# Kernel optimization log

Hardware: AMD Instinct MI355X
Metric: run time of the kernel (lower is better)

Reference implementation:

```python
import jax, jax.numpy as jnp
import numpy as np

NUM_QUERIES = 900
EMBED_DIM = 256
NUM_HEADS = 8
EPS = 1e-5


def bilinear_sample(feats, grid):
    """F.grid_sample(..., align_corners=False, padding_mode='zeros', bilinear).
    feats: [BN, C, H, W], grid: [BN, Q, 2] in [-1,1] (x, y). Returns [BN, Q, C]."""
    BN, C, H, W = feats.shape
    ix = (grid[..., 0] + 1.0) * (W * 0.5) - 0.5
    iy = (grid[..., 1] + 1.0) * (H * 0.5) - 0.5
    x0 = jnp.floor(ix)
    y0 = jnp.floor(iy)
    wx1 = ix - x0
    wy1 = iy - y0
    x0i = x0.astype(jnp.int32)
    y0i = y0.astype(jnp.int32)
    x1i = x0i + 1
    y1i = y0i + 1
    b = jnp.arange(BN)[:, None]

    def gather(yy, xx):
        inb = (xx >= 0) & (xx < W) & (yy >= 0) & (yy < H)
        yc = jnp.clip(yy, 0, H - 1)
        xc = jnp.clip(xx, 0, W - 1)
        v = feats[b, :, yc, xc]  # [BN, Q, C]
        return v * inb[..., None].astype(feats.dtype)

    out = (gather(y0i, x0i) * ((1 - wx1) * (1 - wy1))[..., None]
           + gather(y0i, x1i) * (wx1 * (1 - wy1))[..., None]
           + gather(y1i, x0i) * ((1 - wx1) * wy1)[..., None]
           + gather(y1i, x1i) * (wx1 * wy1)[..., None])
    return out


def setup_inputs() -> dict:
    key = jax.random.key(0)
    ks = jax.random.split(key, 16)
    B, N, C, H, W = 2, 6, 256, 116, 200
    Q, D = NUM_QUERIES, EMBED_DIM
    s = 0.02
    return {
        "image_features": jax.random.normal(ks[0], (B, N, C, H, W), jnp.float32),
        "lidar2img": jax.random.normal(ks[1], (B, N, 4, 4), jnp.float32),
        "query_embedding": jax.random.normal(ks[2], (Q, D), jnp.float32) * s,
        "ref_w": jax.random.normal(ks[3], (3, D), jnp.float32) * s,
        "ref_b": jnp.zeros((3,), jnp.float32),
        "in_proj_w": jax.random.normal(ks[4], (3 * D, D), jnp.float32) * s,
        "in_proj_b": jnp.zeros((3 * D,), jnp.float32),
        "out_proj_w": jax.random.normal(ks[5], (D, D), jnp.float32) * s,
        "out_proj_b": jnp.zeros((D,), jnp.float32),
        "norm_w": jnp.ones((D,), jnp.float32),
        "norm_b": jnp.zeros((D,), jnp.float32),
        "cls_w": jax.random.normal(ks[6], (2, D), jnp.float32) * s,
        "cls_b": jnp.zeros((2,), jnp.float32),
        "box_w": jax.random.normal(ks[7], (6, D), jnp.float32) * s,
        "box_b": jnp.zeros((6,), jnp.float32),
    }


def reference(image_features, lidar2img, query_embedding, ref_w, ref_b,
              in_proj_w, in_proj_b, out_proj_w, out_proj_b,
              norm_w, norm_b, cls_w, cls_b, box_w, box_b):
    B, N, C, H, W = image_features.shape
    Q, D = query_embedding.shape

    q = jnp.broadcast_to(query_embedding[None], (B, Q, D))

    # reference points in [0,1]^3
    ref = jax.nn.sigmoid(q @ ref_w.T + ref_b)  # [B,Q,3]

    # 3D -> 2D projection per camera
    homo = jnp.concatenate([ref, jnp.ones_like(ref[..., :1])], axis=-1)  # [B,Q,4]
    p2h = jnp.einsum('bnij,bqj->bnqi', lidar2img, homo)  # [B,N,Q,4]
    z = p2h[..., 2:3]
    pts2d = p2h[..., 0:2] / (jnp.abs(z) + 1e-5)  # [B,N,Q,2]
    mask = (z > 1e-5)[..., 0]  # [B,N,Q]

    # normalize to [-1,1]
    pn = jnp.stack([pts2d[..., 0] / (W - 1) * 2 - 1,
                    pts2d[..., 1] / (H - 1) * 2 - 1], axis=-1)  # [B,N,Q,2]

    feats_flat = image_features.reshape(B * N, C, H, W)
    grid = pn.reshape(B * N, Q, 2)
    sampled = bilinear_sample(feats_flat, grid)            # [BN,Q,C]
    sampled = sampled.reshape(B, N, Q, C).transpose(0, 2, 1, 3)  # [B,Q,N,C]

    mask_t = mask.transpose(0, 2, 1)[..., None]  # [B,Q,N,1]
    # faithful to torch .view(B,Q,N,2): a raw row-major reshape, not a transpose
    pn_view = pn.reshape(B, Q, N, 2)
    valid = mask_t & (jnp.max(jnp.abs(pn_view), axis=-1, keepdims=True) < 1)  # [B,Q,N,1]
    validf = valid.astype(sampled.dtype)

    sum_feats = jnp.sum(sampled * validf, axis=2)  # [B,Q,C]
    count = jnp.clip(jnp.sum(validf, axis=2), 1.0, None)
    tgt = sum_feats / count

    x = q + tgt  # [B,Q,D]

    # MultiheadAttention (batch_first, 8 heads, no dropout)
    qkv = x @ in_proj_w.T + in_proj_b
    qh, kh, vh = jnp.split(qkv, 3, axis=-1)
    hd = D // NUM_HEADS
    def heads(t):
        return t.reshape(B, Q, NUM_HEADS, hd).transpose(0, 2, 1, 3)  # [B,h,Q,hd]
    qh, kh, vh = heads(qh), heads(kh), heads(vh)
    scores = jnp.einsum('bhqd,bhkd->bhqk', qh, kh) / jnp.sqrt(jnp.asarray(hd, x.dtype))
    attn = jax.nn.softmax(scores, axis=-1)
    o = jnp.einsum('bhqk,bhkd->bhqd', attn, vh).transpose(0, 2, 1, 3).reshape(B, Q, D)
    o = o @ out_proj_w.T + out_proj_b

    # LayerNorm (no residual, faithful to the module)
    mu = jnp.mean(o, axis=-1, keepdims=True)
    var = jnp.mean((o - mu) ** 2, axis=-1, keepdims=True)
    xn = (o - mu) / jnp.sqrt(var + EPS) * norm_w + norm_b

    box = xn @ box_w.T + box_b
    box = jnp.concatenate([jax.nn.sigmoid(box[..., :3]), box[..., 3:]], axis=-1)
    cls = xn @ cls_w.T + cls_b
    return cls, box
```

## Files before the change

### kernel.cpp

```cpp
#include <hip/hip_runtime.h>
#include <math.h>

#define BB 2
#define NCAM 6
#define CC 256
#define HH 116
#define WW 200
#define QQ 900
#define DD 256
#define NHD 8
#define HD 32
#define HWSZ (HH*WW)

__device__ __forceinline__ float sigmoidf_(float x){ return 1.0f/(1.0f+expf(-x)); }

__global__ void ref_kernel(const float* __restrict__ qe, const float* __restrict__ ref_w,
                           const float* __restrict__ ref_b, float* __restrict__ ref) {
    int idx = blockIdx.x*256 + threadIdx.x;
    if (idx >= QQ*3) return;
    int q = idx/3, j = idx%3;
    float acc = ref_b[j];
    const float* qr = qe + q*DD;
    const float* wr = ref_w + j*DD;
    for (int k=0;k<DD;k++) acc += qr[k]*wr[k];
    ref[idx] = sigmoidf_(acc);
}

__global__ void proj_kernel(const float* __restrict__ l2i, const float* __restrict__ ref,
        float* __restrict__ wxa, float* __restrict__ wya,
        int* __restrict__ x0a, int* __restrict__ y0a,
        int* __restrict__ maskz, int* __restrict__ inimg) {
    int idx = blockIdx.x*256+threadIdx.x;
    if (idx >= BB*NCAM*QQ) return;
    int q = idx % QQ;
    int bn = idx / QQ;
    float h0 = ref[q*3+0], h1 = ref[q*3+1], h2 = ref[q*3+2];
    const float* m = l2i + bn*16;
    float px = m[0]*h0+m[1]*h1+m[2]*h2+m[3];
    float py = m[4]*h0+m[5]*h1+m[6]*h2+m[7];
    float pz = m[8]*h0+m[9]*h1+m[10]*h2+m[11];
    float denom = fabsf(pz)+1e-5f;
    float sx = px/denom, sy = py/denom;
    float pnx = sx/(float)(WW-1)*2.0f-1.0f;
    float pny = sy/(float)(HH-1)*2.0f-1.0f;
    maskz[idx] = (pz > 1e-5f) ? 1 : 0;
    inimg[idx] = (fmaxf(fabsf(pnx),fabsf(pny)) < 1.0f) ? 1 : 0;
    float ix = (pnx+1.0f)*(WW*0.5f)-0.5f;
    float iy = (pny+1.0f)*(HH*0.5f)-0.5f;
    float x0f = floorf(ix), y0f = floorf(iy);
    wxa[idx] = ix-x0f; wya[idx] = iy-y0f;
    x0a[idx] = (int)x0f; y0a[idx] = (int)y0f;
}

__global__ __launch_bounds__(256) void sample_kernel(const float* __restrict__ feats,
        const float* __restrict__ qe, const float* __restrict__ wxa, const float* __restrict__ wya,
        const int* __restrict__ x0a, const int* __restrict__ y0a,
        const int* __restrict__ maskz, const int* __restrict__ inimg,
        float* __restrict__ xout) {
    int bq = blockIdx.x;
    int b = bq / QQ, q = bq % QQ;
    int c = threadIdx.x;
    float sum = 0.0f;
    int cnt = 0;
    for (int n = 0; n < NCAM; n++) {
        int s = (b*NCAM+n)*QQ + q;
        int sq = b*(NCAM*QQ) + q*NCAM + n;
        int v = maskz[s] & inimg[sq];
        if (!v) continue;
        cnt++;
        float wx = wxa[s], wy = wya[s];
        int x0 = x0a[s], y0 = y0a[s];
        int x1 = x0+1, y1 = y0+1;
        const float* fb = feats + ((size_t)(b*NCAM+n)*CC + c)*HWSZ;
        float w00 = (1.f-wx)*(1.f-wy), w10 = wx*(1.f-wy), w01 = (1.f-wx)*wy, w11 = wx*wy;
        bool xin0 = ((unsigned)x0 < (unsigned)WW);
        bool xin1 = ((unsigned)x1 < (unsigned)WW);
        if ((unsigned)y0 < (unsigned)HH) {
            const float* row = fb + y0*WW;
            if (xin0) sum += w00*row[x0];
            if (xin1) sum += w10*row[x1];
        }
        if ((unsigned)y1 < (unsigned)HH) {
            const float* row = fb + y1*WW;
            if (xin0) sum += w01*row[x0];
            if (xin1) sum += w11*row[x1];
        }
    }
    float tgt = sum / (float)(cnt > 0 ? cnt : 1);
    xout[(size_t)bq*DD + c] = qe[q*DD+c] + tgt;
}

#define TILE 64
#define BKK 16
__global__ __launch_bounds__(256) void sgemm_nt(const float* __restrict__ A,
        const float* __restrict__ Bw, const float* __restrict__ bias,
        float* __restrict__ Cm, int M, int N, int K) {
    __shared__ float As[BKK][TILE];
    __shared__ float Bs[BKK][TILE];
    int tid = threadIdx.x;
    int m0 = blockIdx.y * TILE, n0 = blockIdx.x * TILE;
    float acc[4][4] = {};
    int tx = tid & 15, ty = tid >> 4;
    for (int k0 = 0; k0 < K; k0 += BKK) {
        #pragma unroll
        for (int i = 0; i < 4; i++) {
            int idx = tid + i * 256;
            int m = idx >> 4;
            int k = idx & 15;
            int gm = m0 + m;
            As[k][m] = (gm < M) ? A[(size_t)gm * K + k0 + k] : 0.0f;
            int gn = n0 + m;
            Bs[k][m] = (gn < N) ? Bw[(size_t)gn * K + k0 + k] : 0.0f;
        }
        __syncthreads();
        #pragma unroll
        for (int k = 0; k < BKK; k++) {
            float a[4], bb[4];
            #pragma unroll
            for (int i = 0; i < 4; i++) a[i] = As[k][ty*4+i];
            #pragma unroll
            for (int j = 0; j < 4; j++) bb[j] = Bs[k][tx*4+j];
            #pragma unroll
            for (int i = 0; i < 4; i++)
                #pragma unroll
                for (int j = 0; j < 4; j++)
                    acc[i][j] += a[i] * bb[j];
        }
        __syncthreads();
    }
    for (int i = 0; i < 4; i++) {
        int gm = m0 + ty*4 + i;
        if (gm >= M) continue;
        for (int j = 0; j < 4; j++) {
            int gn = n0 + tx*4 + j;
            if (gn < N) Cm[(size_t)gm * N + gn] = acc[i][j] + bias[gn];
        }
    }
}

#define QTILE 32
#define KTILE 64
#define NQB 29
__global__ __launch_bounds__(256) void attn_flash(const float* __restrict__ qkv,
                                                  float* __restrict__ attn_out) {
    __shared__ __align__(16) float Qs[32][36];
    __shared__ __align__(16) float Ks[32][68];
    __shared__ __align__(16) float Vs[64][36];
    __shared__ __align__(16) float Ps[32][68];
    int blk = blockIdx.x;
    int qb = blk % NQB;
    int h  = (blk / NQB) % NHD;
    int b  = blk / (NQB*NHD);
    int q0 = qb * QTILE;
    int tid = threadIdx.x;
    int tx = tid & 15, ty = tid >> 4;

    {
        int q = tid >> 3;
        int dseg = (tid & 7) * 4;
        int gq = q0 + q; if (gq > QQ-1) gq = QQ-1;
        const float4 f = *(const float4*)(qkv + ((size_t)(b*QQ+gq))*768 + h*HD + dseg);
        Qs[dseg+0][q] = f.x; Qs[dseg+1][q] = f.y; Qs[dseg+2][q] = f.z; Qs[dseg+3][q] = f.w;
    }

    float O[2][2] = {};
    float l[2] = {0.f, 0.f};
    const float scale = 0.17677669529663689f;

    for (int k0 = 0; k0 < QQ; k0 += KTILE) {
        {
            int k = tid >> 2;
            int dseg = (tid & 3) * 8;
            int gk = k0 + k; if (gk > QQ-1) gk = QQ-1;
            const float* kp = qkv + ((size_t)(b*QQ+gk))*768 + 256 + h*HD + dseg;
            float4 f0 = *(const float4*)(kp);
            float4 f1 = *(const float4*)(kp+4);
            Ks[dseg+0][k]=f0.x; Ks[dseg+1][k]=f0.y; Ks[dseg+2][k]=f0.z; Ks[dseg+3][k]=f0.w;
            Ks[dseg+4][k]=f1.x; Ks[dseg+5][k]=f1.y; Ks[dseg+6][k]=f1.z; Ks[dseg+7][k]=f1.w;
            const float* vp = qkv + ((size_t)(b*QQ+gk))*768 + 512 + h*HD + dseg;
            *(float4*)(&Vs[k][dseg])   = *(const float4*)(vp);
            *(float4*)(&Vs[k][dseg+4]) = *(const float4*)(vp+4);
        }
        __syncthreads();

        float acc[2][4] = {};
        #pragma unroll
        for (int d = 0; d < 32; d++) {
            float a0 = Qs[d][ty*2];
            float a1 = Qs[d][ty*2+1];
            float4 bk = *(const float4*)(&Ks[d][tx*4]);
            acc[0][0] += a0*bk.x; acc[0][1] += a0*bk.y; acc[0][2] += a0*bk.z; acc[0][3] += a0*bk.w;
            acc[1][0] += a1*bk.x; acc[1][1] += a1*bk.y; acc[1][2] += a1*bk.z; acc[1][3] += a1*bk.w;
        }
        #pragma unroll
        for (int i = 0; i < 2; i++) {
            float e[4];
            float rs = 0.f;
            #pragma unroll
            for (int j = 0; j < 4; j++) {
                int gk = k0 + tx*4 + j;
                float v = (gk < QQ) ? expf(acc[i][j]*scale) : 0.f;
                e[j] = v; rs += v;
            }
            #pragma unroll
            for (int m = 1; m < 16; m <<= 1) rs += __shfl_xor(rs, m, 16);
            l[i] += rs;
            *(float4*)(&Ps[ty*2+i][tx*4]) = make_float4(e[0],e[1],e[2],e[3]);
        }
        __syncthreads();

        #pragma unroll
        for (int k4 = 0; k4 < 16; k4++) {
            float4 p0 = *(const float4*)(&Ps[ty*2][k4*4]);
            float4 p1 = *(const float4*)(&Ps[ty*2+1][k4*4]);
            float2 v0 = *(const float2*)(&Vs[k4*4+0][tx*2]);
            float2 v1 = *(const float2*)(&Vs[k4*4+1][tx*2]);
            float2 v2 = *(const float2*)(&Vs[k4*4+2][tx*2]);
            float2 v3 = *(const float2*)(&Vs[k4*4+3][tx*2]);
            O[0][0] += p0.x*v0.x + p0.y*v1.x + p0.z*v2.x + p0.w*v3.x;
            O[0][1] += p0.x*v0.y + p0.y*v1.y + p0.z*v2.y + p0.w*v3.y;
            O[1][0] += p1.x*v0.x + p1.y*v1.x + p1.z*v2.x + p1.w*v3.x;
            O[1][1] += p1.x*v0.y + p1.y*v1.y + p1.z*v2.y + p1.w*v3.y;
        }
        __syncthreads();
    }

    #pragma unroll
    for (int i = 0; i < 2; i++) {
        int gq = q0 + ty*2 + i;
        if (gq < QQ) {
            float inv = 1.0f / l[i];
            float* op = attn_out + ((size_t)(b*QQ+gq))*DD + h*HD + tx*2;
            op[0] = O[i][0]*inv;
            op[1] = O[i][1]*inv;
        }
    }
}

__global__ __launch_bounds__(256) void final_kernel(const float* __restrict__ o,
    const float* __restrict__ norm_w, const float* __restrict__ norm_b,
    const float* __restrict__ cls_w, const float* __restrict__ cls_b,
    const float* __restrict__ box_w, const float* __restrict__ box_b,
    float* __restrict__ out) {
    __shared__ float s_xn[DD];
    __shared__ float red[8];
    int bq = blockIdx.x;
    int t = threadIdx.x;
    float val = o[(size_t)bq*DD + t];
    float v1 = val, v2 = val*val;
    for (int off=32; off>0; off>>=1) { v1 += __shfl_down(v1, off); v2 += __shfl_down(v2, off); }
    if ((t & 63) == 0) { red[t>>6] = v1; red[4 + (t>>6)] = v2; }
    __syncthreads();
    float ssum = red[0]+red[1]+red[2]+red[3];
    float ssq  = red[4]+red[5]+red[6]+red[7];
    float mu = ssum / (float)DD;
    float var = ssq / (float)DD - mu*mu;
    float inv = 1.0f / sqrtf(var + 1e-5f);
    s_xn[t] = (val - mu)*inv*norm_w[t] + norm_b[t];
    __syncthreads();
    int j = t >> 5, lane = t & 31;
    const float* wrow = (j < 2) ? (cls_w + j*DD) : (box_w + (j-2)*DD);
    float acc = 0.f;
    for (int k=lane; k<DD; k+=32) acc += s_xn[k]*wrow[k];
    for (int off=16; off>0; off>>=1) acc += __shfl_down(acc, off, 32);
    if (lane == 0) {
        if (j < 2) {
            out[(size_t)bq*2 + j] = acc + cls_b[j];
        } else {
            int jj = j-2;
            float v = acc + box_b[jj];
            if (jj < 3) v = sigmoidf_(v);
            out[BB*QQ*2 + (size_t)bq*6 + jj] = v;
        }
    }
}

extern "C" void kernel_launch(void* const* d_in, const int* in_sizes, int n_in,
                              void* d_out, int out_size, void* d_ws, size_t ws_size,
                              hipStream_t stream) {
    const float* feats = (const float*)d_in[0];
    const float* l2i   = (const float*)d_in[1];
    const float* qe    = (const float*)d_in[2];
    const float* ref_w = (const float*)d_in[3];
    const float* ref_b = (const float*)d_in[4];
    const float* ipw   = (const float*)d_in[5];
    const float* ipb   = (const float*)d_in[6];
    const float* opw   = (const float*)d_in[7];
    const float* opb   = (const float*)d_in[8];
    const float* nw    = (const float*)d_in[9];
    const float* nb    = (const float*)d_in[10];
    const float* clsw  = (const float*)d_in[11];
    const float* clsb  = (const float*)d_in[12];
    const float* boxw  = (const float*)d_in[13];
    const float* boxb  = (const float*)d_in[14];
    float* out = (float*)d_out;
    float* ws = (float*)d_ws;

    float* ref   = ws;
    float* wxa   = ws + 2700;
    float* wya   = wxa + 10800;
    int*   x0a   = (int*)(wya + 10800);
    int*   y0a   = x0a + 10800;
    int*   maskz = y0a + 10800;
    int*   inimg = maskz + 10800;
    float* x     = (float*)(inimg + 10800);
    float* qkv   = x + 460800;
    float* attn  = qkv + 1382400;
    float* oproj = attn + 460800;

    ref_kernel<<<(QQ*3+255)/256, 256, 0, stream>>>(qe, ref_w, ref_b, ref);
    proj_kernel<<<(BB*NCAM*QQ+255)/256, 256, 0, stream>>>(l2i, ref, wxa, wya, x0a, y0a, maskz, inimg);
    sample_kernel<<<BB*QQ, 256, 0, stream>>>(feats, qe, wxa, wya, x0a, y0a, maskz, inimg, x);
    sgemm_nt<<<dim3(768/TILE, (BB*QQ+TILE-1)/TILE), 256, 0, stream>>>(x, ipw, ipb, qkv, BB*QQ, 768, 256);
    attn_flash<<<BB*NHD*NQB, 256, 0, stream>>>(qkv, attn);
    sgemm_nt<<<dim3(256/TILE, (BB*QQ+TILE-1)/TILE), 256, 0, stream>>>(attn, opw, opb, oproj, BB*QQ, 256, 256);
    final_kernel<<<BB*QQ, 256, 0, stream>>>(oproj, nw, nb, clsw, clsb, boxw, boxb, out);
}
```

Before: 504.9 us.

## Split attention over key halves, vectorize GEMM loads, branchless bilinear sampling

Attention blocks now process half of the key tiles each, writing unnormalized partial outputs and row sums that a new combine kernel merges, doubling grid parallelism; Q is held in registers and fast exp is used. The GEMM tile loads use float4 with padded shared memory, the reference projection uses float4 dot products, and the sampling kernel computes clamped indices with masked weights instead of branches. The split adds an extra kernel launch and extra global traffic for partials, and branchless sampling always issues four loads.

Result: faster. 469.7 us (-7.0%).

```diff
diff --git a/kernel.cpp b/kernel.cpp
--- a/kernel.cpp
+++ b/kernel.cpp
@@ -20,9 +20,12 @@
     if (idx >= QQ*3) return;
     int q = idx/3, j = idx%3;
     float acc = ref_b[j];
-    const float* qr = qe + q*DD;
-    const float* wr = ref_w + j*DD;
-    for (int k=0;k<DD;k++) acc += qr[k]*wr[k];
+    const float4* qr = (const float4*)(qe + q*DD);
+    const float4* wr = (const float4*)(ref_w + j*DD);
+    for (int k=0;k<DD/4;k++) {
+        float4 a = qr[k], w = wr[k];
+        acc += a.x*w.x + a.y*w.y + a.z*w.z + a.w*w.w;
+    }
     ref[idx] = sigmoidf_(acc);
 }
 
@@ -62,6 +65,7 @@
     int c = threadIdx.x;
     float sum = 0.0f;
     int cnt = 0;
+    #pragma unroll
     for (int n = 0; n < NCAM; n++) {
         int s = (b*NCAM+n)*QQ + q;
         int sq = b*(NCAM*QQ) + q*NCAM + n;
@@ -70,21 +74,23 @@
         cnt++;
         float wx = wxa[s], wy = wya[s];
         int x0 = x0a[s], y0 = y0a[s];
-        int x1 = x0+1, y1 = y0+1;
+        int x1 = x0 + 1, y1 = y0 + 1;
+        bool x0in = (unsigned)x0 < (unsigned)WW;
+        bool x1in = (unsigned)x1 < (unsigned)WW;
+        bool y0in = (unsigned)y0 < (unsigned)HH;
+        bool y1in = (unsigned)y1 < (unsigned)HH;
+        int x0c = x0in ? x0 : 0;
+        int x1c = x1in ? x1 : (WW-1);
+        int y0c = y0in ? y0 : 0;
+        int y1c = y1in ? y1 : (HH-1);
+        float w00 = (x0in && y0in) ? (1.f-wx)*(1.f-wy) : 0.f;
+        float w10 = (x1in && y0in) ? wx*(1.f-wy) : 0.f;
+        float w01 = (x0in && y1in) ? (1.f-wx)*wy : 0.f;
+        float w11 = (x1in && y1in) ? wx*wy : 0.f;
         const float* fb = feats + ((size_t)(b*NCAM+n)*CC + c)*HWSZ;
-        float w00 = (1.f-wx)*(1.f-wy), w10 = wx*(1.f-wy), w01 = (1.f-wx)*wy, w11 = wx*wy;
-        bool xin0 = ((unsigned)x0 < (unsigned)WW);
-        bool xin1 = ((unsigned)x1 < (unsigned)WW);
-        if ((unsigned)y0 < (unsigned)HH) {
-            const float* row = fb + y0*WW;
-            if (xin0) sum += w00*row[x0];
-            if (xin1) sum += w10*row[x1];
-        }
-        if ((unsigned)y1 < (unsigned)HH) {
-            const float* row = fb + y1*WW;
-            if (xin0) sum += w01*row[x0];
-            if (xin1) sum += w11*row[x1];
-        }
+        const float* r0 = fb + y0c*WW;
+        const float* r1 = fb + y1c*WW;
+        sum += w00*r0[x0c] + w10*r0[x1c] + w01*r1[x0c] + w11*r1[x1c];
     }
     float tgt = sum / (float)(cnt > 0 ? cnt : 1);
     xout[(size_t)bq*DD + c] = qe[q*DD+c] + tgt;
@@ -95,23 +101,23 @@
 __global__ __launch_bounds__(256) void sgemm_nt(const float* __restrict__ A,
         const float* __restrict__ Bw, const float* __restrict__ bias,
         float* __restrict__ Cm, int M, int N, int K) {
-    __shared__ float As[BKK][TILE];
-    __shared__ float Bs[BKK][TILE];
+    __shared__ float As[BKK][TILE+4];
+    __shared__ float Bs[BKK][TILE+4];
     int tid = threadIdx.x;
     int m0 = blockIdx.y * TILE, n0 = blockIdx.x * TILE;
     float acc[4][4] = {};
     int tx = tid & 15, ty = tid >> 4;
+    int ms = tid >> 2;
+    int kq = (tid & 3) * 4;
     for (int k0 = 0; k0 < K; k0 += BKK) {
-        #pragma unroll
-        for (int i = 0; i < 4; i++) {
-            int idx = tid + i * 256;
-            int m = idx >> 4;
-            int k = idx & 15;
-            int gm = m0 + m;
-            As[k][m] = (gm < M) ? A[(size_t)gm * K + k0 + k] : 0.0f;
-            int gn = n0 + m;
-            Bs[k][m] = (gn < N) ? Bw[(size_t)gn * K + k0 + k] : 0.0f;
-        }
+        int gm = m0 + ms;
+        float4 fa = (gm < M) ? *(const float4*)(A + (size_t)gm * K + k0 + kq)
+                             : make_float4(0.f,0.f,0.f,0.f);
+        As[kq+0][ms]=fa.x; As[kq+1][ms]=fa.y; As[kq+2][ms]=fa.z; As[kq+3][ms]=fa.w;
+        int gn = n0 + ms;
+        float4 fb = (gn < N) ? *(const float4*)(Bw + (size_t)gn * K + k0 + kq)
+                             : make_float4(0.f,0.f,0.f,0.f);
+        Bs[kq+0][ms]=fb.x; Bs[kq+1][ms]=fb.y; Bs[kq+2][ms]=fb.z; Bs[kq+3][ms]=fb.w;
         __syncthreads();
         #pragma unroll
         for (int k = 0; k < BKK; k++) {
@@ -142,15 +148,16 @@
 #define KTILE 64
 #define NQB 29
 __global__ __launch_bounds__(256) void attn_flash(const float* __restrict__ qkv,
-                                                  float* __restrict__ attn_out) {
-    __shared__ __align__(16) float Qs[32][36];
+        float* __restrict__ opA, float* __restrict__ opB,
+        float* __restrict__ lpA, float* __restrict__ lpB) {
     __shared__ __align__(16) float Ks[32][68];
     __shared__ __align__(16) float Vs[64][36];
     __shared__ __align__(16) float Ps[32][68];
     int blk = blockIdx.x;
     int qb = blk % NQB;
     int h  = (blk / NQB) % NHD;
-    int b  = blk / (NQB*NHD);
+    int b  = (blk / (NQB*NHD)) % BB;
+    int ks = blk / (NQB*NHD*BB);
     int q0 = qb * QTILE;
     int tid = threadIdx.x;
     int tx = tid & 15, ty = tid >> 4;
@@ -160,14 +167,22 @@
         int dseg = (tid & 7) * 4;
         int gq = q0 + q; if (gq > QQ-1) gq = QQ-1;
         const float4 f = *(const float4*)(qkv + ((size_t)(b*QQ+gq))*768 + h*HD + dseg);
-        Qs[dseg+0][q] = f.x; Qs[dseg+1][q] = f.y; Qs[dseg+2][q] = f.z; Qs[dseg+3][q] = f.w;
-    }
+        Ps[dseg+0][q] = f.x; Ps[dseg+1][q] = f.y; Ps[dseg+2][q] = f.z; Ps[dseg+3][q] = f.w;
+    }
+    __syncthreads();
+    float q0r[32], q1r[32];
+    #pragma unroll
+    for (int d = 0; d < 32; d++) { q0r[d] = Ps[d][ty*2]; q1r[d] = Ps[d][ty*2+1]; }
+    __syncthreads();
 
     float O[2][2] = {};
     float l[2] = {0.f, 0.f};
     const float scale = 0.17677669529663689f;
-
-    for (int k0 = 0; k0 < QQ; k0 += KTILE) {
+    int kt0 = ks ? 8 : 0;
+    int kt1 = ks ? 15 : 8;
+
+    for (int kt = kt0; kt < kt1; kt++) {
+        int k0 = kt * KTILE;
         {
             int k = tid >> 2;
             int dseg = (tid & 3) * 8;
@@ -186,9 +201,8 @@
         float acc[2][4] = {};
         #pragma unroll
         for (int d = 0; d < 32; d++) {
-            float a0 = Qs[d][ty*2];
-            float a1 = Qs[d][ty*2+1];
             float4 bk = *(const float4*)(&Ks[d][tx*4]);
+            float a0 = q0r[d], a1 = q1r[d];
             acc[0][0] += a0*bk.x; acc[0][1] += a0*bk.y; acc[0][2] += a0*bk.z; acc[0][3] += a0*bk.w;
             acc[1][0] += a1*bk.x; acc[1][1] += a1*bk.y; acc[1][2] += a1*bk.z; acc[1][3] += a1*bk.w;
         }
@@ -199,7 +213,7 @@
             #pragma unroll
             for (int j = 0; j < 4; j++) {
                 int gk = k0 + tx*4 + j;
-                float v = (gk < QQ) ? expf(acc[i][j]*scale) : 0.f;
+                float v = (gk < QQ) ? __expf(acc[i][j]*scale) : 0.f;
                 e[j] = v; rs += v;
             }
             #pragma unroll
@@ -225,16 +239,33 @@
         __syncthreads();
     }
 
+    float* op = ks ? opB : opA;
+    float* lp = ks ? lpB : lpA;
     #pragma unroll
     for (int i = 0; i < 2; i++) {
         int gq = q0 + ty*2 + i;
         if (gq < QQ) {
-            float inv = 1.0f / l[i];
-            float* op = attn_out + ((size_t)(b*QQ+gq))*DD + h*HD + tx*2;
-            op[0] = O[i][0]*inv;
-            op[1] = O[i][1]*inv;
-        }
-    }
+            float* o = op + (((size_t)(b*NHD+h))*QQ + gq)*HD + tx*2;
+            o[0] = O[i][0];
+            o[1] = O[i][1];
+            if (tx == 0) lp[(b*NHD+h)*QQ + gq] = l[i];
+        }
+    }
+}
+
+__global__ __launch_bounds__(256) void attn_combine(const float* __restrict__ opA,
+        const float* __restrict__ opB, const float* __restrict__ lpA,
+        const float* __restrict__ lpB, float* __restrict__ attn_out) {
+    int idx = blockIdx.x*256 + threadIdx.x;
+    if (idx >= BB*QQ*DD) return;
+    int c = idx & 255;
+    int bq = idx >> 8;
+    int b = bq / QQ, q = bq % QQ;
+    int h = c >> 5, d = c & 31;
+    size_t base = ((size_t)(b*NHD+h))*QQ + q;
+    float o = opA[base*HD + d] + opB[base*HD + d];
+    float L = lpA[base] + lpB[base];
+    attn_out[idx] = o / L;
 }
 
 __global__ __launch_bounds__(256) void final_kernel(const float* __restrict__ o,
@@ -308,11 +339,17 @@
     float* attn  = qkv + 1382400;
     float* oproj = attn + 460800;
 
+    float* opA = x;
+    float* opB = oproj;
+    float* lpA = wxa;
+    float* lpB = wxa + 14400;
+
     ref_kernel<<<(QQ*3+255)/256, 256, 0, stream>>>(qe, ref_w, ref_b, ref);
     proj_kernel<<<(BB*NCAM*QQ+255)/256, 256, 0, stream>>>(l2i, ref, wxa, wya, x0a, y0a, maskz, inimg);
     sample_kernel<<<BB*QQ, 256, 0, stream>>>(feats, qe, wxa, wya, x0a, y0a, maskz, inimg, x);
     sgemm_nt<<<dim3(768/TILE, (BB*QQ+TILE-1)/TILE), 256, 0, stream>>>(x, ipw, ipb, qkv, BB*QQ, 768, 256);
-    attn_flash<<<BB*NHD*NQB, 256, 0, stream>>>(qkv, attn);
+    attn_flash<<<BB*NHD*NQB*2, 256, 0, stream>>>(qkv, opA, opB, lpA, lpB);
+    attn_combine<<<(BB*QQ*DD+255)/256, 256, 0, stream>>>(opA, opB, lpA, lpB, attn);
     sgemm_nt<<<dim3(256/TILE, (BB*QQ+TILE-1)/TILE), 256, 0, stream>>>(attn, opw, opb, oproj, BB*QQ, 256, 256);
     final_kernel<<<BB*QQ, 256, 0, stream>>>(oproj, nw, nb, clsw, clsb, boxw, boxb, out);
 }
```
